# Performance work log

Measured on AMD Instinct MI355X. Metric: run time of the kernel, lower is better.

## Reference

```python
import jax, jax.numpy as jnp
import numpy as np

B, D, H, K = 16384, 128, 1024, 8
OPD = 3 * K + 1  # params per dim
TB = 3.0         # tail_bound: left=bottom=-TB, right=top=TB
EPS = 1e-12
MIN_W = MIN_H = MIN_D = 1e-3


def _masks():
    rng = np.random.RandomState(0)
    in_deg = np.arange(1, D + 1)
    h1 = rng.randint(1, D, size=(H,))
    h2 = rng.randint(1, D, size=(H,))
    out_deg = np.arange(1, D + 1)
    m1 = (in_deg[None, :] <= h1[:, None]).astype(np.float32)          # [H, D]
    m2 = (h1[None, :] <= h2[:, None]).astype(np.float32)              # [H, H]
    m3 = np.repeat((out_deg[:, None] > h2[None, :]).astype(np.float32), OPD, axis=0)  # [D*OPD, H]
    return jnp.asarray(m1), jnp.asarray(m2), jnp.asarray(m3)


def _kaiming(key, fan_out, fan_in, a=0.1):
    bound = np.sqrt(6.0 / ((1.0 + a * a) * fan_in))
    return jax.random.uniform(key, (fan_out, fan_in), jnp.float32, -bound, bound)


def setup_inputs() -> dict:
    key = jax.random.key(0)
    kx, k1, k2, k3 = jax.random.split(key, 4)
    m1, m2, m3 = _masks()
    return {
        'x': jax.random.normal(kx, (B, D), jnp.float32),
        'W1': _kaiming(k1, H, D), 'b1': jnp.zeros((H,), jnp.float32),
        'W2': _kaiming(k2, H, H), 'b2': jnp.zeros((H,), jnp.float32),
        'W3': _kaiming(k3, D * OPD, H), 'b3': jnp.zeros((D * OPD,), jnp.float32),
        'm1': m1, 'm2': m2, 'm3': m3,
    }


def _norm_cum(u, mn):
    k = u.shape[-1]
    w = jax.nn.softmax(u, axis=-1)
    w = mn + (1.0 - mn * k) * w
    c = jnp.cumsum(w, axis=-1)
    c = jnp.pad(c, [(0, 0)] * (c.ndim - 1) + [(1, 0)])
    c = c / jnp.clip(c[..., -1:], 1e-12)
    return c[..., 1:] - c[..., :-1], c


def _take(p, idx):
    return jnp.take_along_axis(p, idx[..., None], axis=-1)[..., 0]


def _forward(x, W1, b1, W2, b2, W3, b3, m1, m2, m3):
    h = jax.nn.silu(x @ (W1 * m1).T + b1)
    h = jax.nn.silu(h @ (W2 * m2).T + b2)
    raw = (h @ (W3 * m3).T + b3).reshape(-1, D, OPD)  # [B, D, 3K+1]
    uw, uh, ud = raw[..., :K], raw[..., K:2 * K], raw[..., 2 * K:]
    w, cw = _norm_cum(uw, MIN_W)
    hh, ch = _norm_cum(uh, MIN_H)
    d = MIN_D + jax.nn.softplus(ud)  # [B, D, K+1]

    left, right, bottom, top = -TB, TB, -TB, TB
    inside = (x >= left) & (x <= right)  # [B, D]
    xs = jnp.clip((x - left) / (right - left), 0.0, 1.0)
    bid = jnp.clip(jnp.sum((xs[..., None] >= cw), axis=-1) - 1, 0, K - 1)
    xk, wk = _take(cw, bid), _take(w, bid)
    yk, hk = _take(ch, bid), _take(hh, bid)
    dk, dk1 = _take(d, bid), _take(d, bid + 1)
    t = jnp.clip((xs - xk) / (wk + EPS), 0.0, 1.0)
    a = (hk + EPS) / (wk + EPS)
    num = a * t * t + dk * t * (1 - t)
    den = a + (dk + dk1 - 2 * a) * t * (1 - t)
    s = num / (den + EPS)
    y = (yk + hk * s) * (top - bottom) + bottom
    dnum = a * a * (dk1 * t * t + 2 * a * t * (1 - t) + dk * (1 - t) * (1 - t))
    dydx = (top - bottom) / (right - left) * dnum / (den * den + EPS)
    out = jnp.where(inside, y, x)
    lad = jnp.where(inside, jnp.log(jnp.clip(dydx, 1e-12)), 0.0)
    return out, jnp.sum(lad, axis=-1)


def reference(x, W1, b1, W2, b2, W3, b3, m1, m2, m3):
    return _forward(x, W1, b1, W2, b2, W3, b3, m1, m2, m3)
```

## Files before the change

### kernel.cpp

```cpp
#include <hip/hip_runtime.h>
#include <hip/hip_bf16.h>

#define BATCH 16384
#define DIM   128
#define HID   1024
#define NK    8
#define OPD   25
#define N3    (DIM*OPD)
#define NP    3328

typedef __attribute__((ext_vector_type(8))) short  short8;
typedef __attribute__((ext_vector_type(4))) float  floatx4;
typedef unsigned int u32;

__device__ __forceinline__ float fexp(float x) { return __expf(x); }
__device__ __forceinline__ float flog(float x) { return __logf(x); }
__device__ __forceinline__ float fdiv(float a, float b) { return __fdividef(a, b); }

__device__ __forceinline__ void async_copy16(const unsigned short* g,
                                             unsigned short* l) {
    __builtin_amdgcn_global_load_lds(
        (const __attribute__((address_space(1))) u32*)g,
        (__attribute__((address_space(3))) u32*)l,
        16, 0, 0);
}

__global__ __launch_bounds__(256) void prep_x_lad_kernel(
    const float* __restrict__ x, __hip_bfloat16* __restrict__ xb,
    float* __restrict__ lad) {
    int i = blockIdx.x * 256 + threadIdx.x;
    xb[i] = __float2bfloat16(x[i]);
    if (i < BATCH) lad[i] = 0.f;
}

__global__ __launch_bounds__(128) void hsum_kernel(
    const float* __restrict__ m1, const float* __restrict__ m3,
    int* __restrict__ h1i, int* __restrict__ h2i) {
    const int b = blockIdx.x, t = threadIdx.x;
    if (b < HID) {
        float v = m1[b * DIM + t];
        #pragma unroll
        for (int off = 32; off > 0; off >>= 1) v += __shfl_down(v, off, 64);
        __shared__ float ws[2];
        if ((t & 63) == 0) ws[t >> 6] = v;
        __syncthreads();
        if (t == 0) h1i[b] = (int)(ws[0] + ws[1] + 0.5f);
    } else {
        const int j = (b - HID) * 128 + t;
        float s = 0.f;
        for (int d = 0; d < DIM; d++) s += m3[(size_t)d * OPD * HID + j];
        h2i[j] = DIM - (int)(s + 0.5f);
    }
}

__global__ __launch_bounds__(1024) void sort_kernel(
    const int* __restrict__ h1i, const int* __restrict__ h2i,
    int* __restrict__ perm1, int* __restrict__ perm2,
    int* __restrict__ h1sv, int* __restrict__ h2sv,
    int* __restrict__ klim1, int* __restrict__ klim2, int* __restrict__ klim3)
{
    __shared__ int hist[128];
    __shared__ int h1s[1024], h2s[1024];
    const int t = threadIdx.x;
    const int h1v = h1i[t], h2v = h2i[t];

    if (t < 128) hist[t] = 0;
    __syncthreads();
    atomicAdd(&hist[h1v], 1);
    __syncthreads();
    if (t == 0) { int a = 0; for (int b = 0; b < 128; b++) { int c = hist[b]; hist[b] = a; a += c; } }
    __syncthreads();
    int r = atomicAdd(&hist[h1v], 1);
    perm1[r] = t; h1s[r] = h1v; h1sv[r] = h1v;
    __syncthreads();
    if (t < 128) hist[t] = 0;
    __syncthreads();
    atomicAdd(&hist[h2v], 1);
    __syncthreads();
    if (t == 0) { int a = 0; for (int b = 0; b < 128; b++) { int c = hist[b]; hist[b] = a; a += c; } }
    __syncthreads();
    r = atomicAdd(&hist[h2v], 1);
    perm2[r] = t; h2s[r] = h2v; h2sv[r] = h2v;
    __syncthreads();

    if (t < 8) {
        klim1[t] = ((h1s[t * 128 + 127] + 63) >> 6) << 6;
        int mh = h2s[t * 128 + 127];
        int c = 0;
        for (int j = 0; j < 1024; j++) c += (h1s[j] <= mh) ? 1 : 0;
        klim2[t] = ((c + 63) >> 6) << 6;
    }
    if (t < 26) {
        int dmax = t * 5 + 4; if (dmax > 127) dmax = 127;
        int c = 0;
        for (int j = 0; j < 1024; j++) c += (h2s[j] <= dmax) ? 1 : 0;
        klim3[t] = ((c + 63) >> 6) << 6;
    }
}

__global__ void w1_perm_kernel(const float* __restrict__ W1,
                               const float* __restrict__ b1,
                               const int* __restrict__ perm1,
                               const int* __restrict__ h1sv,
                               __hip_bfloat16* __restrict__ w1p,
                               float* __restrict__ b1p) {
    int i = blockIdx.x * blockDim.x + threadIdx.x;
    int hp = i >> 7, col = i & 127;
    int src = perm1[hp];
    float v = (col < h1sv[hp]) ? W1[src * DIM + col] : 0.f;
    w1p[i] = __float2bfloat16(v);
    if (col == 0) b1p[hp] = b1[src];
}

__global__ __launch_bounds__(256) void w2_perm_kernel(
    const float* __restrict__ W2, const float* __restrict__ b2,
    const int* __restrict__ perm1, const int* __restrict__ perm2,
    const int* __restrict__ h1sv, const int* __restrict__ h2sv,
    __hip_bfloat16* __restrict__ w2p, float* __restrict__ b2p)
{
    __shared__ float row[HID];
    const int ip = blockIdx.x, t = threadIdx.x;
    const int si = perm2[ip];
    const int h2v = h2sv[ip];
    #pragma unroll
    for (int q = 0; q < 4; q++) row[q * 256 + t] = W2[(size_t)si * HID + q * 256 + t];
    __syncthreads();
    #pragma unroll
    for (int q = 0; q < 4; q++) {
        const int jp = q * 256 + t;
        float v = (h1sv[jp] <= h2v) ? row[perm1[jp]] : 0.f;
        w2p[(size_t)ip * HID + jp] = __float2bfloat16(v);
    }
    if (t == 0) b2p[ip] = b2[si];
}

__global__ __launch_bounds__(256) void w3_perm_kernel(
    const float* __restrict__ W3,
    const int* __restrict__ perm2, const int* __restrict__ h2sv,
    __hip_bfloat16* __restrict__ w3p)
{
    __shared__ float row[HID];
    const int c = blockIdx.x, t = threadIdx.x;
    const int s = c & 127, t3 = c >> 7;
    if (s >= 125) {
        #pragma unroll
        for (int q = 0; q < 4; q++)
            w3p[(size_t)c * HID + q * 256 + t] = __float2bfloat16(0.f);
        return;
    }
    const int srcrow = t3 * 125 + s;
    const int d = srcrow / 25;
    #pragma unroll
    for (int q = 0; q < 4; q++) row[q * 256 + t] = W3[(size_t)srcrow * HID + q * 256 + t];
    __syncthreads();
    #pragma unroll
    for (int q = 0; q < 4; q++) {
        const int kk = q * 256 + t;
        float v = (h2sv[kk] <= d) ? row[perm2[kk]] : 0.f;
        w3p[(size_t)c * HID + kk] = __float2bfloat16(v);
    }
}

__device__ __forceinline__ void spline_eval(const float* __restrict__ p,
                                            float xv, float& yout, float& lout) {
    float cw[NK + 1], ch[NK + 1];
    {
        float mx = p[0];
        #pragma unroll
        for (int j = 1; j < NK; j++) mx = fmaxf(mx, p[j]);
        float e[NK], s = 0.f;
        #pragma unroll
        for (int j = 0; j < NK; j++) { e[j] = fexp(p[j] - mx); s += e[j]; }
        const float inv = fdiv(1.f, s);
        cw[0] = 0.f;
        #pragma unroll
        for (int j = 0; j < NK; j++) cw[j + 1] = cw[j] + (0.001f + 0.992f * e[j] * inv);
    }
    {
        float mx = p[8];
        #pragma unroll
        for (int j = 1; j < NK; j++) mx = fmaxf(mx, p[8 + j]);
        float e[NK], s = 0.f;
        #pragma unroll
        for (int j = 0; j < NK; j++) { e[j] = fexp(p[8 + j] - mx); s += e[j]; }
        const float inv = fdiv(1.f, s);
        ch[0] = 0.f;
        #pragma unroll
        for (int j = 0; j < NK; j++) ch[j + 1] = ch[j] + (0.001f + 0.992f * e[j] * inv);
    }
    const float icw = fdiv(1.f, fmaxf(cw[NK], 1e-12f));
    const float ich = fdiv(1.f, fmaxf(ch[NK], 1e-12f));

    const bool inside = (xv >= -3.f) && (xv <= 3.f);
    float xs = (xv + 3.f) * (1.f / 6.f);
    xs = fminf(fmaxf(xs, 0.f), 1.f);
    const float xsc = xs * cw[NK];

    float xk = 0.f, wk = cw[1], yk = 0.f, hk = ch[1];
    float uda = p[16], udb = p[17];
    #pragma unroll
    for (int j = 1; j < NK; j++) {
        const bool c = (xsc >= cw[j]);
        xk  = c ? cw[j] : xk;
        wk  = c ? (cw[j + 1] - cw[j]) : wk;
        yk  = c ? ch[j] : yk;
        hk  = c ? (ch[j + 1] - ch[j]) : hk;
        uda = c ? p[16 + j] : uda;
        udb = c ? p[17 + j] : udb;
    }
    xk *= icw; wk *= icw;
    yk *= ich; hk *= ich;

    const float dk  = 0.001f + ((uda > 20.f) ? uda : flog(1.f + fexp(uda)));
    const float dk1 = 0.001f + ((udb > 20.f) ? udb : flog(1.f + fexp(udb)));

    float t = fdiv(xs - xk, wk + 1e-12f);
    t = fminf(fmaxf(t, 0.f), 1.f);
    const float a   = fdiv(hk + 1e-12f, wk + 1e-12f);
    const float omt = 1.f - t;
    const float tt1 = t * omt;
    const float num = a * t * t + dk * tt1;
    const float den = a + (dk + dk1 - 2.f * a) * tt1;
    const float s   = fdiv(num, den + 1e-12f);
    const float y   = (yk + hk * s) * 6.f - 3.f;
    const float dnum = a * a * (dk1 * t * t + 2.f * a * tt1 + dk * omt * omt);
    const float dydx = fdiv(dnum, den * den + 1e-12f);

    yout = inside ? y : xv;
    lout = inside ? flog(fmaxf(dydx, 1e-12f)) : 0.f;
}

__global__ __launch_bounds__(256, 4) void gemm_bt_kernel(
    const unsigned short* __restrict__ A,
    const unsigned short* __restrict__ Bw,
    const float* __restrict__ bias,
    const int* __restrict__ klim,
    __hip_bfloat16* __restrict__ Cout,
    int M, int N, int Kd)
{
    constexpr int BM = 128, BN = 128, BK = 64;
    __shared__ unsigned short As[BM * BK];
    __shared__ unsigned short Bs[BN * BK];

    const int bid = blockIdx.y * gridDim.x + blockIdx.x;
    const int GY  = (gridDim.y >= 16) ? 16 : gridDim.y;
    const int per_group = gridDim.x * GY;
    const int g  = bid / per_group;
    const int rr = bid % per_group;
    const int bn = (gridDim.x - 1 - rr / GY) * BN;
    const int bm = (g * GY + (rr % GY)) * BM;
    const int Klim = klim[bn >> 7];

    const int t    = threadIdx.x;
    const int lane = t & 63;
    const int w    = t >> 6;
    const int wr   = (w >> 1) * 64;
    const int wc   = (w & 1) * 64;
    const int lr   = lane & 15;
    const int quad = lane >> 4;
    const int lxor = lr & 7;

    floatx4 acc[4][4] = {};

    const int lrow = lane >> 3;
    const int lcol = ((lane & 7) ^ lrow) * 8;

    for (int k0 = 0; k0 < Klim; k0 += BK) {
        __syncthreads();
        #pragma unroll
        for (int p = 0; p < 4; p++) {
            const int q = w * 4 + p;
            const int r = q * 8 + lrow;
            async_copy16(&A[(size_t)(bm + r) * Kd + k0 + lcol],
                         &As[q * 512 + lane * 8]);
            async_copy16(&Bw[(size_t)(bn + r) * Kd + k0 + lcol],
                         &Bs[q * 512 + lane * 8]);
        }
        __syncthreads();
        #pragma unroll
        for (int ks = 0; ks < BK; ks += 32) {
            const int cbase = (ks >> 3) + quad;
            const int coff  = (cbase ^ lxor) * 8;
            short8 af[4], bfr[4];
            #pragma unroll
            for (int i = 0; i < 4; i++)
                af[i] = *(const short8*)&As[(wr + i * 16 + lr) * BK + coff];
            #pragma unroll
            for (int j = 0; j < 4; j++)
                bfr[j] = *(const short8*)&Bs[(wc + j * 16 + lr) * BK + coff];
            #pragma unroll
            for (int i = 0; i < 4; i++)
                #pragma unroll
                for (int j = 0; j < 4; j++)
                    acc[i][j] = __builtin_amdgcn_mfma_f32_16x16x32_bf16(
                        af[i], bfr[j], acc[i][j], 0, 0, 0);
        }
    }

    #pragma unroll
    for (int j = 0; j < 4; j++) {
        const int col = bn + wc + j * 16 + lr;
        const float bv = bias[col];
        #pragma unroll
        for (int i = 0; i < 4; i++) {
            const int rowb = bm + wr + i * 16 + quad * 4;
            #pragma unroll
            for (int r = 0; r < 4; r++) {
                float v = acc[i][j][r] + bv;
                v = v * fdiv(1.f, 1.f + fexp(-v));
                Cout[(size_t)(rowb + r) * N + col] = __float2bfloat16(v);
            }
        }
    }
}

__global__ __launch_bounds__(256, 4) void gemm3_spline_kernel(
    const unsigned short* __restrict__ A,
    const unsigned short* __restrict__ Bw,
    const float* __restrict__ b3,
    const int* __restrict__ klim,
    const float* __restrict__ x,
    float* __restrict__ out,
    float* __restrict__ lad,
    int M)
{
    constexpr int BM = 128, BN = 128, BK = 64, Kd = HID;
    constexpr int LSE = 133;
    __shared__ __align__(16) char smem[64 * LSE * 4 + 128 * 4];
    unsigned short* As = (unsigned short*)smem;
    unsigned short* Bs = (unsigned short*)(smem + BM * BK * 2);
    float* eb     = (float*)smem;
    float* ladacc = (float*)(smem + 64 * LSE * 4);

    const int bid = blockIdx.y * gridDim.x + blockIdx.x;
    const int GY  = 16;
    const int per_group = gridDim.x * GY;
    const int g  = bid / per_group;
    const int rr = bid % per_group;
    const int tile = 25 - rr / GY;
    const int bn = tile * BN;
    const int bm = (g * GY + (rr % GY)) * BM;
    const int Klim = klim[tile];

    const int t    = threadIdx.x;
    const int lane = t & 63;
    const int w    = t >> 6;
    const int wr   = (w >> 1) * 64;
    const int wc   = (w & 1) * 64;
    const int lr   = lane & 15;
    const int quad = lane >> 4;
    const int lxor = lr & 7;

    if (t < 128) ladacc[t] = 0.f;

    floatx4 acc[4][4] = {};

    const int lrow = lane >> 3;
    const int lcol = ((lane & 7) ^ lrow) * 8;

    for (int k0 = 0; k0 < Klim; k0 += BK) {
        __syncthreads();
        #pragma unroll
        for (int p = 0; p < 4; p++) {
            const int q = w * 4 + p;
            const int r = q * 8 + lrow;
            async_copy16(&A[(size_t)(bm + r) * Kd + k0 + lcol],
                         &As[q * 512 + lane * 8]);
            async_copy16(&Bw[(size_t)(bn + r) * Kd + k0 + lcol],
                         &Bs[q * 512 + lane * 8]);
        }
        __syncthreads();
        #pragma unroll
        for (int ks = 0; ks < BK; ks += 32) {
            const int cbase = (ks >> 3) + quad;
            const int coff  = (cbase ^ lxor) * 8;
            short8 af[4], bfr[4];
            #pragma unroll
            for (int i = 0; i < 4; i++)
                af[i] = *(const short8*)&As[(wr + i * 16 + lr) * BK + coff];
            #pragma unroll
            for (int j = 0; j < 4; j++)
                bfr[j] = *(const short8*)&Bs[(wc + j * 16 + lr) * BK + coff];
            #pragma unroll
            for (int i = 0; i < 4; i++)
                #pragma unroll
                for (int j = 0; j < 4; j++)
                    acc[i][j] = __builtin_amdgcn_mfma_f32_16x16x32_bf16(
                        af[i], bfr[j], acc[i][j], 0, 0, 0);
        }
    }

    #pragma unroll 1
    for (int h = 0; h < 2; h++) {
        __syncthreads();
        if ((w >> 1) == h) {
            #pragma unroll
            for (int j = 0; j < 4; j++) {
                const int s = wc + j * 16 + lr;
                const float bv = (s < 125) ? b3[tile * 125 + s] : 0.f;
                #pragma unroll
                for (int i = 0; i < 4; i++) {
                    const int lrw = i * 16 + quad * 4;
                    #pragma unroll
                    for (int r2 = 0; r2 < 4; r2++)
                        eb[(lrw + r2) * LSE + s] = acc[i][j][r2] + bv;
                }
            }
        }
        __syncthreads();
        #pragma unroll 1
        for (int q = t; q < 320; q += 256) {
            const int r  = q / 5;
            const int ds = q % 5;
            const int dim = tile * 5 + ds;
            if (dim < DIM) {
                const float* p = eb + r * LSE + ds * 25;
                const int grow = bm + h * 64 + r;
                const float xv = x[(size_t)grow * DIM + dim];
                float y, l;
                spline_eval(p, xv, y, l);
                out[(size_t)grow * DIM + dim] = y;
                atomicAdd(&ladacc[h * 64 + r], l);
            }
        }
    }
    __syncthreads();
    if (t < 128) atomicAdd(&lad[bm + t], ladacc[t]);
}

extern "C" void kernel_launch(void* const* d_in, const int* in_sizes, int n_in,
                              void* d_out, int out_size, void* d_ws, size_t ws_size,
                              hipStream_t stream) {
    const float* x  = (const float*)d_in[0];
    const float* W1 = (const float*)d_in[1];
    const float* b1 = (const float*)d_in[2];
    const float* W2 = (const float*)d_in[3];
    const float* b2 = (const float*)d_in[4];
    const float* W3 = (const float*)d_in[5];
    const float* b3 = (const float*)d_in[6];
    const float* m1 = (const float*)d_in[7];
    const float* m3 = (const float*)d_in[9];

    char* ws = (char*)d_ws;
    const size_t OFF_W1B = 0;
    const size_t OFF_W2B = OFF_W1B + (size_t)HID * DIM * 2;
    const size_t OFF_W3P = OFF_W2B + (size_t)HID * HID * 2;
    const size_t OFF_XB  = OFF_W3P + (size_t)NP * HID * 2;
    const size_t OFF_H1B = OFF_XB  + (size_t)BATCH * DIM * 2;
    const size_t OFF_H2B = OFF_H1B + (size_t)BATCH * HID * 2;
    const size_t OFF_SML = OFF_H2B + (size_t)BATCH * HID * 2;

    __hip_bfloat16* w1p = (__hip_bfloat16*)(ws + OFF_W1B);
    __hip_bfloat16* w2p = (__hip_bfloat16*)(ws + OFF_W2B);
    __hip_bfloat16* w3p = (__hip_bfloat16*)(ws + OFF_W3P);
    __hip_bfloat16* xb  = (__hip_bfloat16*)(ws + OFF_XB);
    __hip_bfloat16* h1b = (__hip_bfloat16*)(ws + OFF_H1B);
    __hip_bfloat16* h2b = (__hip_bfloat16*)(ws + OFF_H2B);

    float* b1p   = (float*)(ws + OFF_SML);
    float* b2p   = b1p + HID;
    int*   h1i   = (int*)(b2p + HID);
    int*   h2i   = h1i + HID;
    int*   perm1 = h2i + HID;
    int*   perm2 = perm1 + HID;
    int*   h1sv  = perm2 + HID;
    int*   h2sv  = h1sv + HID;
    int*   klim1 = h2sv + HID;
    int*   klim2 = klim1 + 8;
    int*   klim3 = klim2 + 8;

    float* out_p = (float*)d_out;
    float* lad_p = out_p + (size_t)BATCH * DIM;

    hsum_kernel<<<HID + 8, 128, 0, stream>>>(m1, m3, h1i, h2i);
    sort_kernel<<<1, 1024, 0, stream>>>(h1i, h2i, perm1, perm2, h1sv, h2sv,
                                        klim1, klim2, klim3);
    w1_perm_kernel<<<(HID * DIM) / 256, 256, 0, stream>>>(W1, b1, perm1, h1sv,
                                                          w1p, b1p);
    w2_perm_kernel<<<HID, 256, 0, stream>>>(W2, b2, perm1, perm2, h1sv, h2sv,
                                            w2p, b2p);
    w3_perm_kernel<<<NP, 256, 0, stream>>>(W3, perm2, h2sv, w3p);
    prep_x_lad_kernel<<<(BATCH * DIM) / 256, 256, 0, stream>>>(x, xb, lad_p);

    gemm_bt_kernel<<<dim3(HID / 128, BATCH / 128), 256, 0, stream>>>(
        (const unsigned short*)xb, (const unsigned short*)w1p, b1p, klim1, h1b,
        BATCH, HID, DIM);
    gemm_bt_kernel<<<dim3(HID / 128, BATCH / 128), 256, 0, stream>>>(
        (const unsigned short*)h1b, (const unsigned short*)w2p, b2p, klim2, h2b,
        BATCH, HID, HID);
    gemm3_spline_kernel<<<dim3(NP / 128, BATCH / 128), 256, 0, stream>>>(
        (const unsigned short*)h2b, (const unsigned short*)w3p, b3, klim3, x,
        out_p, lad_p, BATCH);
}
```

Measured before the change: 287.5 us.

## Double-buffer GEMM K-loop with async LDS staging and merge weight prep kernels

Replaces the single-buffered BK=64 K-loop in both GEMM kernels with a two-slot BK=32 ping-pong pipeline: the next slot's global-to-LDS async copy is issued before computing on the current slot, using a new swizzle. This is meant to hide global load latency behind MFMA work. The four weight/input preparation kernels are also merged into one launch to cut launch overhead. The spline epilogue shrinks its LDS stride and moves ladacc zeroing after the loop, since the shared memory now aliases the double buffers. The risk is extra barriers per K step.

```diff
diff --git a/kernel.cpp b/kernel.cpp
--- a/kernel.cpp
+++ b/kernel.cpp
@@ -25,13 +25,58 @@
         16, 0, 0);
 }
 
-__global__ __launch_bounds__(256) void prep_x_lad_kernel(
-    const float* __restrict__ x, __hip_bfloat16* __restrict__ xb,
-    float* __restrict__ lad) {
-    int i = blockIdx.x * 256 + threadIdx.x;
-    xb[i] = __float2bfloat16(x[i]);
-    if (i < BATCH) lad[i] = 0.f;
-}
+__device__ __forceinline__ void stage_slot(const unsigned short* __restrict__ A,
+                                           const unsigned short* __restrict__ Bw,
+                                           unsigned short* As, unsigned short* Bs,
+                                           size_t abase, size_t bbase,
+                                           int Kd, int kc, int w, int lane) {
+    const int rsub = lane >> 2;
+    const int csw  = ((lane & 3) ^ ((lane >> 3) & 3)) * 8;
+    #pragma unroll
+    for (int p = 0; p < 2; p++) {
+        const int q = w * 2 + p;
+        async_copy16(&A[abase + (size_t)(q * 16 + rsub) * Kd + kc + csw],
+                     &As[q * 512 + lane * 8]);
+        async_copy16(&Bw[bbase + (size_t)(q * 16 + rsub) * Kd + kc + csw],
+                     &Bs[q * 512 + lane * 8]);
+    }
+}
+
+__device__ __forceinline__ void compute_slot(const unsigned short* As,
+                                             const unsigned short* Bs,
+                                             int wr, int wc, int lr, int quad,
+                                             floatx4 acc[4][4]) {
+    const int csel = (quad ^ ((lr >> 1) & 3)) * 8;
+    short8 af[4], bfr[4];
+    #pragma unroll
+    for (int i = 0; i < 4; i++)
+        af[i] = *(const short8*)&As[(wr + i * 16 + lr) * 32 + csel];
+    #pragma unroll
+    for (int j = 0; j < 4; j++)
+        bfr[j] = *(const short8*)&Bs[(wc + j * 16 + lr) * 32 + csel];
+    #pragma unroll
+    for (int i = 0; i < 4; i++)
+        #pragma unroll
+        for (int j = 0; j < 4; j++)
+            acc[i][j] = __builtin_amdgcn_mfma_f32_16x16x32_bf16(
+                af[i], bfr[j], acc[i][j], 0, 0, 0);
+}
+
+#define KLOOP_DB(A_, B_, abase_, bbase_, Kd_, Klim_)                          \
+    if (Klim_ > 0) {                                                          \
+        stage_slot(A_, B_, As0, Bs0, abase_, bbase_, Kd_, 0, w, lane);        \
+        for (int k0 = 0; k0 < Klim_; k0 += 64) {                              \
+            asm volatile("s_waitcnt vmcnt(0) lgkmcnt(0)" ::: "memory");       \
+            __builtin_amdgcn_s_barrier();                                     \
+            stage_slot(A_, B_, As1, Bs1, abase_, bbase_, Kd_, k0 + 32, w, lane);\
+            compute_slot(As0, Bs0, wr, wc, lr, quad, acc);                    \
+            asm volatile("s_waitcnt vmcnt(0) lgkmcnt(0)" ::: "memory");       \
+            __builtin_amdgcn_s_barrier();                                     \
+            if (k0 + 64 < Klim_)                                              \
+                stage_slot(A_, B_, As0, Bs0, abase_, bbase_, Kd_, k0 + 64, w, lane);\
+            compute_slot(As1, Bs1, wr, wc, lr, quad, acc);                    \
+        }                                                                     \
+    }
 
 __global__ __launch_bounds__(128) void hsum_kernel(
     const float* __restrict__ m1, const float* __restrict__ m3,
@@ -98,66 +143,64 @@
     }
 }
 
-__global__ void w1_perm_kernel(const float* __restrict__ W1,
-                               const float* __restrict__ b1,
-                               const int* __restrict__ perm1,
-                               const int* __restrict__ h1sv,
-                               __hip_bfloat16* __restrict__ w1p,
-                               float* __restrict__ b1p) {
-    int i = blockIdx.x * blockDim.x + threadIdx.x;
-    int hp = i >> 7, col = i & 127;
-    int src = perm1[hp];
-    float v = (col < h1sv[hp]) ? W1[src * DIM + col] : 0.f;
-    w1p[i] = __float2bfloat16(v);
-    if (col == 0) b1p[hp] = b1[src];
-}
-
-__global__ __launch_bounds__(256) void w2_perm_kernel(
+__global__ __launch_bounds__(256) void wperm_kernel(
+    const float* __restrict__ W1, const float* __restrict__ b1,
     const float* __restrict__ W2, const float* __restrict__ b2,
+    const float* __restrict__ W3, const float* __restrict__ x,
     const int* __restrict__ perm1, const int* __restrict__ perm2,
     const int* __restrict__ h1sv, const int* __restrict__ h2sv,
-    __hip_bfloat16* __restrict__ w2p, float* __restrict__ b2p)
+    __hip_bfloat16* __restrict__ w1p, float* __restrict__ b1p,
+    __hip_bfloat16* __restrict__ w2p, float* __restrict__ b2p,
+    __hip_bfloat16* __restrict__ w3p,
+    __hip_bfloat16* __restrict__ xb, float* __restrict__ lad)
 {
     __shared__ float row[HID];
-    const int ip = blockIdx.x, t = threadIdx.x;
-    const int si = perm2[ip];
-    const int h2v = h2sv[ip];
-    #pragma unroll
-    for (int q = 0; q < 4; q++) row[q * 256 + t] = W2[(size_t)si * HID + q * 256 + t];
-    __syncthreads();
-    #pragma unroll
-    for (int q = 0; q < 4; q++) {
-        const int jp = q * 256 + t;
-        float v = (h1sv[jp] <= h2v) ? row[perm1[jp]] : 0.f;
-        w2p[(size_t)ip * HID + jp] = __float2bfloat16(v);
-    }
-    if (t == 0) b2p[ip] = b2[si];
-}
-
-__global__ __launch_bounds__(256) void w3_perm_kernel(
-    const float* __restrict__ W3,
-    const int* __restrict__ perm2, const int* __restrict__ h2sv,
-    __hip_bfloat16* __restrict__ w3p)
-{
-    __shared__ float row[HID];
-    const int c = blockIdx.x, t = threadIdx.x;
-    const int s = c & 127, t3 = c >> 7;
-    if (s >= 125) {
-        #pragma unroll
-        for (int q = 0; q < 4; q++)
-            w3p[(size_t)c * HID + q * 256 + t] = __float2bfloat16(0.f);
-        return;
-    }
-    const int srcrow = t3 * 125 + s;
-    const int d = srcrow / 25;
-    #pragma unroll
-    for (int q = 0; q < 4; q++) row[q * 256 + t] = W3[(size_t)srcrow * HID + q * 256 + t];
-    __syncthreads();
-    #pragma unroll
-    for (int q = 0; q < 4; q++) {
-        const int kk = q * 256 + t;
-        float v = (h2sv[kk] <= d) ? row[perm2[kk]] : 0.f;
-        w3p[(size_t)c * HID + kk] = __float2bfloat16(v);
+    const int b = blockIdx.x, t = threadIdx.x;
+    if (b < 512) {
+        const int i = b * 256 + t;
+        const int hp = i >> 7, col = i & 127;
+        const int src = perm1[hp];
+        float v = (col < h1sv[hp]) ? W1[src * DIM + col] : 0.f;
+        w1p[i] = __float2bfloat16(v);
+        if (col == 0) b1p[hp] = b1[src];
+    } else if (b < 512 + HID) {
+        const int ip = b - 512;
+        const int si = perm2[ip];
+        const int h2v = h2sv[ip];
+        #pragma unroll
+        for (int q = 0; q < 4; q++) row[q * 256 + t] = W2[(size_t)si * HID + q * 256 + t];
+        __syncthreads();
+        #pragma unroll
+        for (int q = 0; q < 4; q++) {
+            const int jp = q * 256 + t;
+            float v = (h1sv[jp] <= h2v) ? row[perm1[jp]] : 0.f;
+            w2p[(size_t)ip * HID + jp] = __float2bfloat16(v);
+        }
+        if (t == 0) b2p[ip] = b2[si];
+    } else if (b < 512 + HID + NP) {
+        const int c = b - 512 - HID;
+        const int s = c & 127, t3 = c >> 7;
+        if (s >= 125) {
+            #pragma unroll
+            for (int q = 0; q < 4; q++)
+                w3p[(size_t)c * HID + q * 256 + t] = __float2bfloat16(0.f);
+            return;
+        }
+        const int srcrow = t3 * 125 + s;
+        const int d = srcrow / 25;
+        #pragma unroll
+        for (int q = 0; q < 4; q++) row[q * 256 + t] = W3[(size_t)srcrow * HID + q * 256 + t];
+        __syncthreads();
+        #pragma unroll
+        for (int q = 0; q < 4; q++) {
+            const int kk = q * 256 + t;
+            float v = (h2sv[kk] <= d) ? row[perm2[kk]] : 0.f;
+            w3p[(size_t)c * HID + kk] = __float2bfloat16(v);
+        }
+    } else {
+        const int i = (b - (512 + HID + NP)) * 256 + t;
+        xb[i] = __float2bfloat16(x[i]);
+        if (i < BATCH) lad[i] = 0.f;
     }
 }
 
@@ -238,17 +281,19 @@
     __hip_bfloat16* __restrict__ Cout,
     int M, int N, int Kd)
 {
-    constexpr int BM = 128, BN = 128, BK = 64;
-    __shared__ unsigned short As[BM * BK];
-    __shared__ unsigned short Bs[BN * BK];
+    __shared__ __align__(16) unsigned short sm[16384];
+    unsigned short* const As0 = sm;
+    unsigned short* const As1 = sm + 4096;
+    unsigned short* const Bs0 = sm + 8192;
+    unsigned short* const Bs1 = sm + 12288;
 
     const int bid = blockIdx.y * gridDim.x + blockIdx.x;
     const int GY  = (gridDim.y >= 16) ? 16 : gridDim.y;
     const int per_group = gridDim.x * GY;
     const int g  = bid / per_group;
     const int rr = bid % per_group;
-    const int bn = (gridDim.x - 1 - rr / GY) * BN;
-    const int bm = (g * GY + (rr % GY)) * BM;
+    const int bn = (gridDim.x - 1 - rr / GY) * 128;
+    const int bm = (g * GY + (rr % GY)) * 128;
     const int Klim = klim[bn >> 7];
 
     const int t    = threadIdx.x;
@@ -258,44 +303,12 @@
     const int wc   = (w & 1) * 64;
     const int lr   = lane & 15;
     const int quad = lane >> 4;
-    const int lxor = lr & 7;
 
     floatx4 acc[4][4] = {};
-
-    const int lrow = lane >> 3;
-    const int lcol = ((lane & 7) ^ lrow) * 8;
-
-    for (int k0 = 0; k0 < Klim; k0 += BK) {
-        __syncthreads();
-        #pragma unroll
-        for (int p = 0; p < 4; p++) {
-            const int q = w * 4 + p;
-            const int r = q * 8 + lrow;
-            async_copy16(&A[(size_t)(bm + r) * Kd + k0 + lcol],
-                         &As[q * 512 + lane * 8]);
-            async_copy16(&Bw[(size_t)(bn + r) * Kd + k0 + lcol],
-                         &Bs[q * 512 + lane * 8]);
-        }
-        __syncthreads();
-        #pragma unroll
-        for (int ks = 0; ks < BK; ks += 32) {
-            const int cbase = (ks >> 3) + quad;
-            const int coff  = (cbase ^ lxor) * 8;
-            short8 af[4], bfr[4];
-            #pragma unroll
-            for (int i = 0; i < 4; i++)
-                af[i] = *(const short8*)&As[(wr + i * 16 + lr) * BK + coff];
-            #pragma unroll
-            for (int j = 0; j < 4; j++)
-                bfr[j] = *(const short8*)&Bs[(wc + j * 16 + lr) * BK + coff];
-            #pragma unroll
-            for (int i = 0; i < 4; i++)
-                #pragma unroll
-                for (int j = 0; j < 4; j++)
-                    acc[i][j] = __builtin_amdgcn_mfma_f32_16x16x32_bf16(
-                        af[i], bfr[j], acc[i][j], 0, 0, 0);
-        }
-    }
+    const size_t abase = (size_t)bm * Kd;
+    const size_t bbase = (size_t)bn * Kd;
+
+    KLOOP_DB(A, Bw, abase, bbase, Kd, Klim)
 
     #pragma unroll
     for (int j = 0; j < 4; j++) {
@@ -324,11 +337,14 @@
     float* __restrict__ lad,
     int M)
 {
-    constexpr int BM = 128, BN = 128, BK = 64, Kd = HID;
-    constexpr int LSE = 133;
+    constexpr int Kd  = HID;
+    constexpr int LSE = 126;
     __shared__ __align__(16) char smem[64 * LSE * 4 + 128 * 4];
-    unsigned short* As = (unsigned short*)smem;
-    unsigned short* Bs = (unsigned short*)(smem + BM * BK * 2);
+    unsigned short* const sm  = (unsigned short*)smem;
+    unsigned short* const As0 = sm;
+    unsigned short* const As1 = sm + 4096;
+    unsigned short* const Bs0 = sm + 8192;
+    unsigned short* const Bs1 = sm + 12288;
     float* eb     = (float*)smem;
     float* ladacc = (float*)(smem + 64 * LSE * 4);
 
@@ -338,8 +354,8 @@
     const int g  = bid / per_group;
     const int rr = bid % per_group;
     const int tile = 25 - rr / GY;
-    const int bn = tile * BN;
-    const int bm = (g * GY + (rr % GY)) * BM;
+    const int bn = tile * 128;
+    const int bm = (g * GY + (rr % GY)) * 128;
     const int Klim = klim[tile];
 
     const int t    = threadIdx.x;
@@ -349,61 +365,31 @@
     const int wc   = (w & 1) * 64;
     const int lr   = lane & 15;
     const int quad = lane >> 4;
-    const int lxor = lr & 7;
-
-    if (t < 128) ladacc[t] = 0.f;
 
     floatx4 acc[4][4] = {};
-
-    const int lrow = lane >> 3;
-    const int lcol = ((lane & 7) ^ lrow) * 8;
-
-    for (int k0 = 0; k0 < Klim; k0 += BK) {
-        __syncthreads();
-        #pragma unroll
-        for (int p = 0; p < 4; p++) {
-            const int q = w * 4 + p;
-            const int r = q * 8 + lrow;
-            async_copy16(&A[(size_t)(bm + r) * Kd + k0 + lcol],
-                         &As[q * 512 + lane * 8]);
-            async_copy16(&Bw[(size_t)(bn + r) * Kd + k0 + lcol],
-                         &Bs[q * 512 + lane * 8]);
-        }
-        __syncthreads();
-        #pragma unroll
-        for (int ks = 0; ks < BK; ks += 32) {
-            const int cbase = (ks >> 3) + quad;
-            const int coff  = (cbase ^ lxor) * 8;
-            short8 af[4], bfr[4];
-            #pragma unroll
-            for (int i = 0; i < 4; i++)
-                af[i] = *(const short8*)&As[(wr + i * 16 + lr) * BK + coff];
-            #pragma unroll
-            for (int j = 0; j < 4; j++)
-                bfr[j] = *(const short8*)&Bs[(wc + j * 16 + lr) * BK + coff];
-            #pragma unroll
-            for (int i = 0; i < 4; i++)
-                #pragma unroll
-                for (int j = 0; j < 4; j++)
-                    acc[i][j] = __builtin_amdgcn_mfma_f32_16x16x32_bf16(
-                        af[i], bfr[j], acc[i][j], 0, 0, 0);
-        }
-    }
+    const size_t abase = (size_t)bm * Kd;
+    const size_t bbase = (size_t)bn * Kd;
+
+    KLOOP_DB(A, Bw, abase, bbase, Kd, Klim)
 
     #pragma unroll 1
     for (int h = 0; h < 2; h++) {
         __syncthreads();
+        if (h == 0 && t < 128) ladacc[t] = 0.f;
         if ((w >> 1) == h) {
             #pragma unroll
             for (int j = 0; j < 4; j++) {
                 const int s = wc + j * 16 + lr;
-                const float bv = (s < 125) ? b3[tile * 125 + s] : 0.f;
-                #pragma unroll
-                for (int i = 0; i < 4; i++) {
-                    const int lrw = i * 16 + quad * 4;
+                if (s < 125) {
+                    const int bidx = tile * 125 + s;
+                    const float bv = b3[bidx < N3 ? bidx : 0];
                     #pragma unroll
-                    for (int r2 = 0; r2 < 4; r2++)
-                        eb[(lrw + r2) * LSE + s] = acc[i][j][r2] + bv;
+                    for (int i = 0; i < 4; i++) {
+                        const int lrw = i * 16 + quad * 4;
+                        #pragma unroll
+                        for (int r2 = 0; r2 < 4; r2++)
+                            eb[(lrw + r2) * LSE + s] = acc[i][j][r2] + bv;
+                    }
                 }
             }
         }
@@ -475,12 +461,9 @@
     hsum_kernel<<<HID + 8, 128, 0, stream>>>(m1, m3, h1i, h2i);
     sort_kernel<<<1, 1024, 0, stream>>>(h1i, h2i, perm1, perm2, h1sv, h2sv,
                                         klim1, klim2, klim3);
-    w1_perm_kernel<<<(HID * DIM) / 256, 256, 0, stream>>>(W1, b1, perm1, h1sv,
-                                                          w1p, b1p);
-    w2_perm_kernel<<<HID, 256, 0, stream>>>(W2, b2, perm1, perm2, h1sv, h2sv,
-                                            w2p, b2p);
-    w3_perm_kernel<<<NP, 256, 0, stream>>>(W3, perm2, h2sv, w3p);
-    prep_x_lad_kernel<<<(BATCH * DIM) / 256, 256, 0, stream>>>(x, xb, lad_p);
+    wperm_kernel<<<512 + HID + NP + (BATCH * DIM) / 256, 256, 0, stream>>>(
+        W1, b1, W2, b2, W3, x, perm1, perm2, h1sv, h2sv,
+        w1p, b1p, w2p, b2p, w3p, xb, lad_p);
 
     gemm_bt_kernel<<<dim3(HID / 128, BATCH / 128), 256, 0, stream>>>(
         (const unsigned short*)xb, (const unsigned short*)w1p, b1p, klim1, h1b,
```

After: 277.4 us. -3.5%, faster.
